# Optimization experiments

Hardware: AMD Instinct MI355X
Metric: run time of the kernel (lower is better)

## Reference

```python
import jax, jax.numpy as jnp
import numpy as np

W_KERNEL = 5      # dilation kernel size (w)
K_BG = 0.1        # background weight (k)
RELAX = 5.0       # sigmoid temperature (relax)
INF = 1e4         # 'no zero in column' sentinel (>> image diagonal)
EPS = 1e-7        # DiceLoss eps


def setup_inputs() -> dict:
    key = jax.random.key(0)
    k1, k2 = jax.random.split(key)
    B, H, W = 32, 256, 256
    preds = jax.random.normal(k1, (B, H, W), dtype=jnp.float32)
    targets = (jax.random.uniform(k2, (B, H, W)) > 0.99).astype(jnp.float32)
    return {"preds": preds, "targets": targets}


def _dilate(t, w):
    # cv2.dilate with w x w ones kernel == sliding-window max, SAME padding
    pad = w // 2
    return jax.lax.reduce_window(t, -jnp.inf, jax.lax.max,
                                 (1, w, w), (1, 1, 1),
                                 [(0, 0), (pad, pad), (pad, pad)])


def _vertical_dist(zero_mask):
    # per-column distance (in rows) to nearest zero pixel; [B,H,W] -> [B,H,W]
    B, H, W = zero_mask.shape
    rows = jnp.moveaxis(zero_mask, 1, 0)  # [H,B,W]

    def step(carry, z):
        d = jnp.where(z, 0.0, jnp.minimum(carry + 1.0, INF))
        return d, d

    init = jnp.full((B, W), INF, dtype=jnp.float32)
    _, fwd = jax.lax.scan(step, init, rows)
    _, bwd = jax.lax.scan(step, init, rows[::-1])
    g = jnp.minimum(fwd, bwd[::-1])  # [H,B,W]
    return jnp.moveaxis(g, 0, 1)


def _edt(fat):
    # exact euclidean distance transform (distance to nearest zero pixel),
    # separable two-pass: vertical 1D distance, then horizontal min-plus.
    B, H, W = fat.shape
    g = _vertical_dist(fat == 0)  # [B,H,W]
    col = jnp.arange(W, dtype=jnp.float32)
    off2 = (col[:, None] - col[None, :]) ** 2  # [W_j, W_k]

    def per_img(gi):  # gi: [H,W]
        # d2[i,j] = min_k g[i,k]^2 + (j-k)^2   -> [H,W,W] intermediate
        d2 = jnp.min(gi[:, None, :] ** 2 + off2[None, :, :], axis=-1)
        return jnp.sqrt(d2)

    return jax.lax.map(per_img, g)  # sequential over batch caps memory


def _distance_maps(targets):
    fat = _dilate(targets, W_KERNEL)          # [B,H,W]
    d = _edt(fat)                              # [B,H,W]
    soft = jax.nn.sigmoid(d / RELAX)
    soft = soft - jnp.min(soft, axis=(1, 2), keepdims=True)
    mx = jnp.max(soft, axis=(1, 2), keepdims=True)
    soft = soft / jnp.where(mx > 0, mx, 1.0)
    dm_soft = soft + (1.0 - fat) * K_BG
    has_fg = jnp.max(targets, axis=(1, 2), keepdims=True) > 0
    return jnp.where(has_fg, dm_soft, 1.0 - targets)


def reference(preds, targets):
    p = jax.nn.sigmoid(preds)
    dm = jax.lax.stop_gradient(_distance_maps(targets))  # computed in numpy in torch => constant
    pw = p * dm
    bs = pw.shape[0]
    y_pred = pw.reshape(bs, 1, -1)
    y_true = targets.reshape(bs, 1, -1)
    # smp DiceLoss('binary', from_logits=False): dims=(0,2), smooth=0, eps=1e-7
    inter = jnp.sum(y_pred * y_true, axis=(0, 2))
    card = jnp.sum(y_pred + y_true, axis=(0, 2))
    dice = (2.0 * inter) / jnp.maximum(card, EPS)
    loss = 1.0 - dice
    mask = (jnp.sum(y_true, axis=(0, 2)) > 0).astype(loss.dtype)
    return jnp.mean(loss * mask)
```

## Files before the change

kernel.cpp:

```cpp
#include <hip/hip_runtime.h>
#include <math.h>

#define BB 32
#define HH 256
#define WW 256
#define HW (HH*WW)
#define K_BG 0.1f
#define RELAX 5.0f
#define EPS_D 1e-7
#define RPB 8
#define RPT 4
#define MEGA_BLOCKS (BB * (HH / RPB))
#define GP 8

typedef unsigned long long u64;

__device__ __forceinline__ float sigf(float x) {
    float e = __builtin_amdgcn_exp2f(-1.44269504f * x);
    return __builtin_amdgcn_rcpf(1.0f + e);
}

__device__ __forceinline__ u64 shflx64(u64 x, int s) {
    return (u64)__shfl_xor((unsigned long long)x, s, 64);
}

__global__ void k_maskdil(const float* __restrict__ tg, u64* __restrict__ dmaskT,
                          u64* __restrict__ nzmask, unsigned* __restrict__ cnt) {
    __shared__ u64 nz[20][4];
    __shared__ u64 hd[20][4];
    int blk = blockIdx.x;
    int b = blk >> 4, band = blk & 15;
    int r0 = band * 16;
    int t = threadIdx.x, w = t >> 6;
    const float* img = tg + b * HW;
    if (blk == 0 && t == 0) cnt[0] = 0;
    float v[20];
    #pragma unroll
    for (int rr = 0; rr < 20; ++rr) {
        int rg = r0 + rr - 2;
        v[rr] = (rg >= 0 && rg < HH) ? img[rg * WW + t] : 0.0f;
    }
    #pragma unroll
    for (int rr = 0; rr < 20; ++rr) {
        u64 bal = __ballot(v[rr] != 0.0f);
        if ((t & 63) == 0) nz[rr][w] = bal;
    }
    __syncthreads();
    if (t < 80) {
        int rr = t >> 2, k = t & 3;
        u64 m = nz[rr][k];
        u64 ml = (k > 0) ? nz[rr][k - 1] : 0ULL;
        u64 mr = (k < 3) ? nz[rr][k + 1] : 0ULL;
        hd[rr][k] = m | (m << 1) | (m << 2) | (m >> 1) | (m >> 2)
                  | (ml >> 62) | (ml >> 63) | (mr << 62) | (mr << 63);
    }
    if (t < 64) {
        int rr = t >> 2, k = t & 3;
        nzmask[b * 1024 + (r0 + rr) * 4 + k] = nz[rr + 2][k];
    }
    __syncthreads();
    if (t < 64) {
        int rr = t >> 2, k = t & 3;
        u64 o = hd[rr][k] | hd[rr + 1][k] | hd[rr + 2][k] | hd[rr + 3][k] | hd[rr + 4][k];
        dmaskT[b * 1024 + k * 256 + (r0 + rr)] = o;
    }
}

__global__ __launch_bounds__(512, 8) void k_mega(const float* __restrict__ preds,
                                                 const u64* __restrict__ dmaskT,
                                                 const u64* __restrict__ nzmask,
                                                 float4* __restrict__ part1,
                                                 float4* __restrict__ part2,
                                                 unsigned* __restrict__ cnt,
                                                 float* __restrict__ out) {
    __shared__ u64 colT[4 * 256];
    __shared__ float gS[RPB][WW + 2 * GP];
    __shared__ float red[8][8];
    __shared__ unsigned stick;
    __shared__ float sI[BB], sC[BB], sA[BB];
    int blk = blockIdx.x;
    int b = blk >> 5, q = blk & 31;
    int i0 = q * RPB;
    int tid = threadIdx.x;
    int lane = tid & 63, wv = tid >> 6;
    int j = tid & 255;
    int r0t = (tid >> 8) * RPT;

    float p[RPT];
    #pragma unroll
    for (int rr = 0; rr < RPT; ++rr)
        p[rr] = preds[(b * HH + i0 + r0t + rr) * WW + j];
    int wj = j >> 6;
    u64 nzw[RPT];
    #pragma unroll
    for (int rr = 0; rr < RPT; ++rr)
        nzw[rr] = nzmask[b * 1024 + (i0 + r0t + rr) * 4 + wj];

    if (tid < 128) {
        int rr = tid >> 4, c = tid & 15;
        gS[rr][(c < 8) ? c : (c + 256)] = 1e4f;
    }

    const u64* base = dmaskT + b * 1024;
    const u64 L32 = 0x00000000FFFFFFFFULL, L16 = 0x0000FFFF0000FFFFULL,
              L8  = 0x00FF00FF00FF00FFULL, L4  = 0x0F0F0F0F0F0F0F0FULL,
              L2  = 0x3333333333333333ULL, L1  = 0x5555555555555555ULL;
    int tg_ = wv & 3, w0 = (wv >> 2) * 2;
    #pragma unroll
    for (int dw = 0; dw < 2; ++dw) {
        int w = w0 + dw;
        u64 x = base[w * 256 + tg_ * 64 + lane];
        u64 pp;
        pp = shflx64(x, 32); x = (lane & 32) ? ((x & ~L32) | ((pp & ~L32) >> 32)) : ((x & L32) | ((pp & L32) << 32));
        pp = shflx64(x, 16); x = (lane & 16) ? ((x & ~L16) | ((pp & ~L16) >> 16)) : ((x & L16) | ((pp & L16) << 16));
        pp = shflx64(x,  8); x = (lane &  8) ? ((x & ~L8 ) | ((pp & ~L8 ) >>  8)) : ((x & L8 ) | ((pp & L8 ) <<  8));
        pp = shflx64(x,  4); x = (lane &  4) ? ((x & ~L4 ) | ((pp & ~L4 ) >>  4)) : ((x & L4 ) | ((pp & L4 ) <<  4));
        pp = shflx64(x,  2); x = (lane &  2) ? ((x & ~L2 ) | ((pp & ~L2 ) >>  2)) : ((x & L2 ) | ((pp & L2 ) <<  2));
        pp = shflx64(x,  1); x = (lane &  1) ? ((x & ~L1 ) | ((pp & ~L1 ) >>  1)) : ((x & L1 ) | ((pp & L1 ) <<  1));
        colT[tg_ * 256 + w * 64 + lane] = x;
    }
    __syncthreads();

    u64 yw[4];
    #pragma unroll
    for (int g = 0; g < 4; ++g) yw[g] = ~colT[g * 256 + j];

    int g0v[RPT], fgv[RPT], needw[RPT];
    #pragma unroll
    for (int rr = 0; rr < RPT; ++rr) {
        int i = i0 + r0t + rr;
        int iw = i >> 6, ib = i & 63;
        int fg = (int)((~yw[iw] >> ib) & 1ULL);
        fgv[rr] = fg;
        u64 anyf = __ballot(fg != 0);
        needw[rr] = (anyf != 0ULL);
        int g0 = 0;
        if (anyf) {
            u64 lowm  = (2ULL << ib) - 1ULL;
            u64 highm = ~((1ULL << ib) - 1ULL);
            int pu = -1, pd = -1;
            #pragma unroll
            for (int w = 0; w < 4; ++w) {
                u64 m = (w < iw) ? ~0ULL : ((w == iw) ? lowm : 0ULL);
                u64 z = yw[w] & m;
                int cand = (w << 6) + 63 - __clzll(z);
                pu = z ? cand : pu;
            }
            #pragma unroll
            for (int w = 3; w >= 0; --w) {
                u64 m = (w > iw) ? ~0ULL : ((w == iw) ? highm : 0ULL);
                u64 z = yw[w] & m;
                int cand = (w << 6) + (__ffsll((unsigned long long)z) - 1);
                pd = z ? cand : pd;
            }
            int up = (pu >= 0) ? (i - pu) : 10000;
            int dn = (pd >= 0) ? (pd - i) : 10000;
            g0 = min(min(up, dn), 10000);
        }
        g0v[rr] = g0;
        gS[r0t + rr][GP + j] = (float)g0;
    }
    __syncthreads();

    float vals[8];
    #pragma unroll
    for (int qq = 0; qq < 6; ++qq) vals[qq] = 0.0f;
    vals[6] = 1e30f; vals[7] = 0.0f;
    #pragma unroll
    for (int rr = 0; rr < RPT; ++rr) {
        int rt = r0t + rr;
        const float* gr = &gS[rt][GP + j];
        float gv = (float)g0v[rr];
        float best = gv * gv;
        if (needw[rr]) {
            #pragma unroll
            for (int r = 1; r <= 4; ++r) {
                float rf = (float)(r * r);
                float vl = gr[-r], vr = gr[r];
                best = fminf(best, fminf(fmaf(vl, vl, rf), fmaf(vr, vr, rf)));
            }
            for (int rc = 5; rc < WW + 8; rc += 8) {
                if ((float)(rc * rc) >= best) break;
                #pragma unroll
                for (int dr = 0; dr < 8; ++dr) {
                    int r = rc + dr;
                    float rf = (float)(r * r);
                    int jl = j - r, jr = j + r;
                    float vl = (jl >= 0) ? gr[-r] : 1e4f;
                    float vr = (jr < WW) ? gr[r] : 1e4f;
                    best = fminf(best, fminf(fmaf(vl, vl, rf), fmaf(vr, vr, rf)));
                }
            }
        }
        float dv = __builtin_amdgcn_sqrtf(best);
        float sp = sigf(p[rr]);
        float sd = sigf(dv * (1.0f / RELAX));
        float tv = (float)((nzw[rr] >> (j & 63)) & 1ULL);
        vals[0] += sp * sd * tv;
        vals[1] += sp * tv;
        vals[2] += sp * sd;
        vals[3] += sp;
        vals[4] += fgv[rr] ? 0.0f : sp;
        vals[5] += tv;
        vals[6] = fminf(vals[6], dv);
        vals[7] = fmaxf(vals[7], dv);
    }
    for (int off = 32; off > 0; off >>= 1) {
        #pragma unroll
        for (int qq = 0; qq < 6; ++qq) vals[qq] += __shfl_down(vals[qq], off, 64);
        vals[6] = fminf(vals[6], __shfl_down(vals[6], off, 64));
        vals[7] = fmaxf(vals[7], __shfl_down(vals[7], off, 64));
    }
    if (lane == 0) {
        #pragma unroll
        for (int qq = 0; qq < 8; ++qq) red[qq][wv] = vals[qq];
    }
    __syncthreads();
    if (tid == 0) {
        float s[8];
        #pragma unroll
        for (int qq = 0; qq < 6; ++qq) {
            s[qq] = 0.0f;
            #pragma unroll
            for (int k = 0; k < 8; ++k) s[qq] += red[qq][k];
        }
        s[6] = red[6][0]; s[7] = red[7][0];
        #pragma unroll
        for (int k = 1; k < 8; ++k) {
            s[6] = fminf(s[6], red[6][k]);
            s[7] = fmaxf(s[7], red[7][k]);
        }
        part1[blk] = make_float4(s[0], s[1], s[2], s[3]);
        part2[blk] = make_float4(s[4], s[5], s[6], s[7]);
        __threadfence();
        stick = atomicAdd(&cnt[0], 1u);
    }
    __syncthreads();
    if (stick != MEGA_BLOCKS - 1) return;

    __threadfence();
    #pragma unroll
    for (int pass = 0; pass < 2; ++pass) {
        int img = pass * 16 + (tid >> 5);
        int k = tid & 31;
        float4 p1 = part1[img * 32 + k];
        float4 p2 = part2[img * 32 + k];
        float v2[8] = {p1.x, p1.y, p1.z, p1.w, p2.x, p2.y, p2.z, p2.w};
        for (int off = 16; off > 0; off >>= 1) {
            #pragma unroll
            for (int qq = 0; qq < 6; ++qq) v2[qq] += __shfl_down(v2[qq], off, 32);
            v2[6] = fminf(v2[6], __shfl_down(v2[6], off, 32));
            v2[7] = fmaxf(v2[7], __shfl_down(v2[7], off, 32));
        }
        if (k == 0) {
            float A = v2[0], Bs = v2[1], Ap = v2[2], Bp = v2[3];
            float Cp = v2[4], T = v2[5], dmn = v2[6], dmx = v2[7];
            float inter, card, any;
            if (T > 0.0f) {
                float smin = sigf(dmn * (1.0f / RELAX));
                float smax = sigf(dmx * (1.0f / RELAX));
                float m = smax - smin;
                float denom = (m > 0.0f) ? m : 1.0f;
                inter = (A - smin * Bs) / denom;
                card  = (Ap - smin * Bp) / denom + K_BG * Cp + T;
                any = 1.0f;
            } else {
                inter = 0.0f;
                card = Bp - Bs + T;
                any = 0.0f;
            }
            sI[img] = inter; sC[img] = card; sA[img] = any;
        }
    }
    __syncthreads();
    if (tid == 0) {
        double I = 0.0, C = 0.0;
        int any = 0;
        for (int bb = 0; bb < BB; ++bb) {
            I += (double)sI[bb]; C += (double)sC[bb];
            any |= (sA[bb] > 0.0f);
        }
        double dice = 2.0 * I / fmax(C, (double)EPS_D);
        out[0] = any ? (float)(1.0 - dice) : 0.0f;
    }
}

extern "C" void kernel_launch(void* const* d_in, const int* in_sizes, int n_in,
                              void* d_out, int out_size, void* d_ws, size_t ws_size,
                              hipStream_t stream) {
    const float* preds = (const float*)d_in[0];
    const float* tg    = (const float*)d_in[1];
    float* out = (float*)d_out;

    u64* dmaskT   = (u64*)d_ws;
    u64* nzmask   = dmaskT + BB * 1024;
    float4* part1 = (float4*)(nzmask + BB * 1024);
    float4* part2 = part1 + MEGA_BLOCKS;
    unsigned* cnt = (unsigned*)(part2 + MEGA_BLOCKS);

    hipLaunchKernelGGL(k_maskdil, dim3(BB * 16), dim3(WW), 0, stream,
                       tg, dmaskT, nzmask, cnt);
    hipLaunchKernelGGL(k_mega, dim3(MEGA_BLOCKS), dim3(512), 0, stream,
                       preds, dmaskT, nzmask, part1, part2, cnt, out);
}
```

Baseline: 93.78 us.

## Hoist bit-transpose into separate kernel and add fast local vertical-distance path

Moves the per-block 64x64 bit-matrix transpose of the dilated mask out of the main kernel into a small pre-pass kernel that writes a column-major mask once per image. Before, each of 32 blocks per image redid the transpose and synchronised through shared memory. The main kernel now reads the column words directly, which drops one shared array and one barrier. It also computes the vertical distance from the current and neighbouring 64-bit words with ffs/clz, and falls back to the full four-word scan only when the wave contains pixels with no zero nearby. The cost is an extra kernel launch and extra workspace memory traffic.

```diff
diff --git a/kernel.cpp b/kernel.cpp
--- a/kernel.cpp
+++ b/kernel.cpp
@@ -66,14 +66,33 @@
     }
 }
 
+__global__ __launch_bounds__(256) void k_trans(const u64* __restrict__ dmaskT,
+                                               u64* __restrict__ colmask) {
+    int blk = blockIdx.x;
+    int b = blk >> 2, g = blk & 3;
+    int tid = threadIdx.x;
+    int lane = tid & 63, w = tid >> 6;
+    const u64 L32 = 0x00000000FFFFFFFFULL, L16 = 0x0000FFFF0000FFFFULL,
+              L8  = 0x00FF00FF00FF00FFULL, L4  = 0x0F0F0F0F0F0F0F0FULL,
+              L2  = 0x3333333333333333ULL, L1  = 0x5555555555555555ULL;
+    u64 x = dmaskT[b * 1024 + w * 256 + g * 64 + lane];
+    u64 pp;
+    pp = shflx64(x, 32); x = (lane & 32) ? ((x & ~L32) | ((pp & ~L32) >> 32)) : ((x & L32) | ((pp & L32) << 32));
+    pp = shflx64(x, 16); x = (lane & 16) ? ((x & ~L16) | ((pp & ~L16) >> 16)) : ((x & L16) | ((pp & L16) << 16));
+    pp = shflx64(x,  8); x = (lane &  8) ? ((x & ~L8 ) | ((pp & ~L8 ) >>  8)) : ((x & L8 ) | ((pp & L8 ) <<  8));
+    pp = shflx64(x,  4); x = (lane &  4) ? ((x & ~L4 ) | ((pp & ~L4 ) >>  4)) : ((x & L4 ) | ((pp & L4 ) <<  4));
+    pp = shflx64(x,  2); x = (lane &  2) ? ((x & ~L2 ) | ((pp & ~L2 ) >>  2)) : ((x & L2 ) | ((pp & L2 ) <<  2));
+    pp = shflx64(x,  1); x = (lane &  1) ? ((x & ~L1 ) | ((pp & ~L1 ) >>  1)) : ((x & L1 ) | ((pp & L1 ) <<  1));
+    colmask[b * 1024 + g * 256 + w * 64 + lane] = x;
+}
+
 __global__ __launch_bounds__(512, 8) void k_mega(const float* __restrict__ preds,
-                                                 const u64* __restrict__ dmaskT,
+                                                 const u64* __restrict__ colmask,
                                                  const u64* __restrict__ nzmask,
                                                  float4* __restrict__ part1,
                                                  float4* __restrict__ part2,
                                                  unsigned* __restrict__ cnt,
                                                  float* __restrict__ out) {
-    __shared__ u64 colT[4 * 256];
     __shared__ float gS[RPB][WW + 2 * GP];
     __shared__ float red[8][8];
     __shared__ unsigned stick;
@@ -95,68 +114,58 @@
     #pragma unroll
     for (int rr = 0; rr < RPT; ++rr)
         nzw[rr] = nzmask[b * 1024 + (i0 + r0t + rr) * 4 + wj];
+    u64 yw[4];
+    #pragma unroll
+    for (int g = 0; g < 4; ++g)
+        yw[g] = ~colmask[b * 1024 + g * 256 + j];
 
     if (tid < 128) {
         int rr = tid >> 4, c = tid & 15;
         gS[rr][(c < 8) ? c : (c + 256)] = 1e4f;
     }
 
-    const u64* base = dmaskT + b * 1024;
-    const u64 L32 = 0x00000000FFFFFFFFULL, L16 = 0x0000FFFF0000FFFFULL,
-              L8  = 0x00FF00FF00FF00FFULL, L4  = 0x0F0F0F0F0F0F0F0FULL,
-              L2  = 0x3333333333333333ULL, L1  = 0x5555555555555555ULL;
-    int tg_ = wv & 3, w0 = (wv >> 2) * 2;
-    #pragma unroll
-    for (int dw = 0; dw < 2; ++dw) {
-        int w = w0 + dw;
-        u64 x = base[w * 256 + tg_ * 64 + lane];
-        u64 pp;
-        pp = shflx64(x, 32); x = (lane & 32) ? ((x & ~L32) | ((pp & ~L32) >> 32)) : ((x & L32) | ((pp & L32) << 32));
-        pp = shflx64(x, 16); x = (lane & 16) ? ((x & ~L16) | ((pp & ~L16) >> 16)) : ((x & L16) | ((pp & L16) << 16));
-        pp = shflx64(x,  8); x = (lane &  8) ? ((x & ~L8 ) | ((pp & ~L8 ) >>  8)) : ((x & L8 ) | ((pp & L8 ) <<  8));
-        pp = shflx64(x,  4); x = (lane &  4) ? ((x & ~L4 ) | ((pp & ~L4 ) >>  4)) : ((x & L4 ) | ((pp & L4 ) <<  4));
-        pp = shflx64(x,  2); x = (lane &  2) ? ((x & ~L2 ) | ((pp & ~L2 ) >>  2)) : ((x & L2 ) | ((pp & L2 ) <<  2));
-        pp = shflx64(x,  1); x = (lane &  1) ? ((x & ~L1 ) | ((pp & ~L1 ) >>  1)) : ((x & L1 ) | ((pp & L1 ) <<  1));
-        colT[tg_ * 256 + w * 64 + lane] = x;
-    }
-    __syncthreads();
-
-    u64 yw[4];
-    #pragma unroll
-    for (int g = 0; g < 4; ++g) yw[g] = ~colT[g * 256 + j];
-
     int g0v[RPT], fgv[RPT], needw[RPT];
     #pragma unroll
     for (int rr = 0; rr < RPT; ++rr) {
         int i = i0 + r0t + rr;
         int iw = i >> 6, ib = i & 63;
-        int fg = (int)((~yw[iw] >> ib) & 1ULL);
+        u64 cur = yw[iw];
+        u64 nxt = (iw < 3) ? yw[iw + 1] : 0ULL;
+        u64 prv = (iw > 0) ? yw[iw - 1] : 0ULL;
+        u64 dnbits = (cur >> ib) | ((nxt << 1) << (63 - ib));
+        u64 upbits = (cur << (63 - ib)) | ((prv >> 1) >> ib);
+        int fg = (int)(1ULL & ~dnbits);
         fgv[rr] = fg;
+        int dn = dnbits ? (__ffsll((unsigned long long)dnbits) - 1) : 10000;
+        int up = upbits ? __clzll((long long)upbits) : 10000;
+        int g0 = min(dn, up);
+        u64 needfull = __ballot(dnbits == 0ULL && upbits == 0ULL);
+        if (needfull) {
+            if (dnbits == 0ULL && upbits == 0ULL) {
+                u64 lowm  = (2ULL << ib) - 1ULL;
+                u64 highm = ~((1ULL << ib) - 1ULL);
+                int pu = -1, pd = -1;
+                #pragma unroll
+                for (int w = 0; w < 4; ++w) {
+                    u64 m = (w < iw) ? ~0ULL : ((w == iw) ? lowm : 0ULL);
+                    u64 z = yw[w] & m;
+                    int cand = (w << 6) + 63 - __clzll(z);
+                    pu = z ? cand : pu;
+                }
+                #pragma unroll
+                for (int w = 3; w >= 0; --w) {
+                    u64 m = (w > iw) ? ~0ULL : ((w == iw) ? highm : 0ULL);
+                    u64 z = yw[w] & m;
+                    int cand = (w << 6) + (__ffsll((unsigned long long)z) - 1);
+                    pd = z ? cand : pd;
+                }
+                int upf = (pu >= 0) ? (i - pu) : 10000;
+                int dnf = (pd >= 0) ? (pd - i) : 10000;
+                g0 = min(min(upf, dnf), 10000);
+            }
+        }
         u64 anyf = __ballot(fg != 0);
         needw[rr] = (anyf != 0ULL);
-        int g0 = 0;
-        if (anyf) {
-            u64 lowm  = (2ULL << ib) - 1ULL;
-            u64 highm = ~((1ULL << ib) - 1ULL);
-            int pu = -1, pd = -1;
-            #pragma unroll
-            for (int w = 0; w < 4; ++w) {
-                u64 m = (w < iw) ? ~0ULL : ((w == iw) ? lowm : 0ULL);
-                u64 z = yw[w] & m;
-                int cand = (w << 6) + 63 - __clzll(z);
-                pu = z ? cand : pu;
-            }
-            #pragma unroll
-            for (int w = 3; w >= 0; --w) {
-                u64 m = (w > iw) ? ~0ULL : ((w == iw) ? highm : 0ULL);
-                u64 z = yw[w] & m;
-                int cand = (w << 6) + (__ffsll((unsigned long long)z) - 1);
-                pd = z ? cand : pd;
-            }
-            int up = (pu >= 0) ? (i - pu) : 10000;
-            int dn = (pd >= 0) ? (pd - i) : 10000;
-            g0 = min(min(up, dn), 10000);
-        }
         g0v[rr] = g0;
         gS[r0t + rr][GP + j] = (float)g0;
     }
@@ -294,12 +303,15 @@
 
     u64* dmaskT   = (u64*)d_ws;
     u64* nzmask   = dmaskT + BB * 1024;
-    float4* part1 = (float4*)(nzmask + BB * 1024);
+    u64* colmask  = nzmask + BB * 1024;
+    float4* part1 = (float4*)(colmask + BB * 1024);
     float4* part2 = part1 + MEGA_BLOCKS;
     unsigned* cnt = (unsigned*)(part2 + MEGA_BLOCKS);
 
     hipLaunchKernelGGL(k_maskdil, dim3(BB * 16), dim3(WW), 0, stream,
                        tg, dmaskT, nzmask, cnt);
+    hipLaunchKernelGGL(k_trans, dim3(BB * 4), dim3(256), 0, stream,
+                       dmaskT, colmask);
     hipLaunchKernelGGL(k_mega, dim3(MEGA_BLOCKS), dim3(512), 0, stream,
-                       preds, dmaskT, nzmask, part1, part2, cnt, out);
-}
+                       preds, colmask, nzmask, part1, part2, cnt, out);
+}
```

Result: slower. 95.88 us (+2.2%).
